# Kernel tuning notes

Measured on AMD Instinct MI355X. Metric: run time of the kernel, lower is better.

The kernel has to match this reference:

```python
import jax, jax.numpy as jnp
import numpy as np

N_KPS = 1024      # number of TPS control points
N_PTS = 120000    # number of query points to warp
RELAX = 0.5       # TPS relaxation (regularization on K diagonal)


def setup_inputs() -> dict:
    key = jax.random.key(0)
    k1, k2, k3 = jax.random.split(key, 3)
    # Control points in a [0,100)^2 coordinate frame.
    kps_a = jax.random.uniform(k1, (N_KPS, 2), dtype=jnp.float32) * 100.0
    kps_b = kps_a + jax.random.normal(k2, (N_KPS, 2), dtype=jnp.float32) * 2.0
    # --- replicate __init__: solve the TPS system for W ---
    d2 = jnp.sum((kps_a[:, None, :] - kps_a[None, :, :]) ** 2, axis=-1)  # [n_a, n_a]
    d2 = jnp.where(d2 == 0, 1.0, d2)
    K = 0.5 * d2 * jnp.log(d2) + RELAX * jnp.eye(N_KPS, dtype=jnp.float32)
    P = jnp.concatenate([jnp.ones((N_KPS, 1), jnp.float32), kps_a], axis=1)  # [n_a, 3]
    L = jnp.block([[K, P], [P.T, jnp.zeros((3, 3), jnp.float32)]])           # [n_a+3, n_a+3]
    v = jnp.concatenate([kps_b - kps_a, jnp.zeros((3, 2), jnp.float32)], axis=0)
    W = jnp.linalg.solve(L, v)  # [n_a+3, 2]  (equivalent to L.inverse() @ v)
    # Query points
    pts = jax.random.uniform(k3, (N_PTS, 2), dtype=jnp.float32) * 100.0
    return {"pts": pts, "kps_a": kps_a, "W": W}


def reference(pts, kps_a, W):
    # pairwise squared distances, [n_a, n_b] (matches __build_l2_mat)
    l2 = jnp.sum((kps_a[:, None, :] - pts[None, :, :]) ** 2, axis=-1)
    l2 = jnp.where(l2 == 0, 1.0, l2)
    v = 0.5 * l2 * jnp.log(l2)  # TPS radial basis r^2 * log(r)
    ones = jnp.ones_like(pts[:, 0])
    affine = jnp.stack([ones, pts[:, 0], pts[:, 1]], axis=0)   # [3, n_b]
    x = jnp.concatenate([v, affine], axis=0)                   # [n_a+3, n_b]
    z = x.T @ W                                                # [n_b, 2]
    return pts + z
```

## Files before the change

### kernel.cpp

```cpp
#include <hip/hip_runtime.h>

#define N_KPS 1024
#define N_PTS 120000
#define BLOCK 256
#define KSPLIT 4
#define KCHUNK (N_KPS / KSPLIT)
#define PTS_PER_BLOCK 128

typedef float v2f __attribute__((ext_vector_type(2)));

__global__ __launch_bounds__(BLOCK) void tps_warp_kernel(
    const float2* __restrict__ pts,
    const float*  __restrict__ kps,
    const float*  __restrict__ W,
    float2*       __restrict__ out)
{
    __shared__ float4 part[KSPLIT][64];

    const int lane = threadIdx.x & 63;
    const int kch  = threadIdx.x >> 6;
    const int base = blockIdx.x * PTS_PER_BLOCK;
    const int j0 = base + lane;
    const int j1 = base + 64 + lane;

    const int j0c = j0 < N_PTS ? j0 : N_PTS - 1;
    const int j1c = j1 < N_PTS ? j1 : N_PTS - 1;
    const float2 p0 = pts[j0c];
    const float2 p1 = pts[j1c];

    v2f px = {p0.x, p1.x};
    v2f py = {p0.y, p1.y};
    v2f zx = {0.0f, 0.0f};
    v2f zy = {0.0f, 0.0f};
    const v2f tiny = {1e-37f, 1e-37f};

    const int k0 = kch * KCHUNK;
    #pragma unroll 4
    for (int i = k0; i < k0 + KCHUNK; ++i) {
        float kx = kps[2 * i];
        float ky = kps[2 * i + 1];
        float wx = W[2 * i];
        float wy = W[2 * i + 1];
        v2f kxv = {kx, kx}, kyv = {ky, ky};
        v2f wxv = {wx, wx}, wyv = {wy, wy};

        v2f dx = kxv - px;
        v2f dy = kyv - py;
        v2f d2 = __builtin_elementwise_fma(dy, dy, dx * dx);
        d2 = __builtin_elementwise_max(d2, tiny);
        v2f t;
        t.x = __log2f(d2.x);
        t.y = __log2f(d2.y);
        v2f v = d2 * t;
        zx = __builtin_elementwise_fma(v, wxv, zx);
        zy = __builtin_elementwise_fma(v, wyv, zy);
    }

    part[kch][lane] = make_float4(zx.x, zy.x, zx.y, zy.y);
    __syncthreads();

    if (kch == 0) {
        float4 a = part[0][lane];
        float4 b = part[1][lane];
        float4 c = part[2][lane];
        float4 d = part[3][lane];
        float sx0 = (a.x + b.x) + (c.x + d.x);
        float sy0 = (a.y + b.y) + (c.y + d.y);
        float sx1 = (a.z + b.z) + (c.z + d.z);
        float sy1 = (a.w + b.w) + (c.w + d.w);

        const float scale = 0.34657359027997264f;
        float w1x = W[2048], w1y = W[2049];
        float wxx = W[2050], wxy = W[2051];
        float wyx = W[2052], wyy = W[2053];

        if (j0 < N_PTS) {
            float ox = p0.x + fmaf(scale, sx0, fmaf(wxx, p0.x, fmaf(wyx, p0.y, w1x)));
            float oy = p0.y + fmaf(scale, sy0, fmaf(wxy, p0.x, fmaf(wyy, p0.y, w1y)));
            out[j0] = make_float2(ox, oy);
        }
        if (j1 < N_PTS) {
            float ox = p1.x + fmaf(scale, sx1, fmaf(wxx, p1.x, fmaf(wyx, p1.y, w1x)));
            float oy = p1.y + fmaf(scale, sy1, fmaf(wxy, p1.x, fmaf(wyy, p1.y, w1y)));
            out[j1] = make_float2(ox, oy);
        }
    }
}

extern "C" void kernel_launch(void* const* d_in, const int* in_sizes, int n_in,
                              void* d_out, int out_size, void* d_ws, size_t ws_size,
                              hipStream_t stream) {
    const float* pts = (const float*)d_in[0];
    const float* kps = (const float*)d_in[1];
    const float* W   = (const float*)d_in[2];
    float* out = (float*)d_out;

    const int grid = (N_PTS + PTS_PER_BLOCK - 1) / PTS_PER_BLOCK;
    tps_warp_kernel<<<grid, BLOCK, 0, stream>>>(
        (const float2*)pts, kps, W, (float2*)out);
}
```

Measured before the change: 88.39 us.

## Split keypoints across 8 waves with wave-uniform float4 prefetched loads

Doubles the block to 512 threads so eight waves each handle 128 keypoints, and makes the wave index scalar via readfirstlane. Keypoint and weight data are now read as float4 vectors through scalar loads and double-buffered one chunk ahead of use, to cut per-iteration load latency and instruction count. The final reduction sums eight partial results instead of four. Larger blocks may lower occupancy flexibility and add more LDS reduction work per point.

```diff
diff --git a/kernel.cpp b/kernel.cpp
--- a/kernel.cpp
+++ b/kernel.cpp
@@ -2,10 +2,12 @@
 
 #define N_KPS 1024
 #define N_PTS 120000
-#define BLOCK 256
-#define KSPLIT 4
+#define BLOCK 512
+#define KSPLIT 8
 #define KCHUNK (N_KPS / KSPLIT)
 #define PTS_PER_BLOCK 128
+#define CHUNK 8
+#define NCHUNK (KCHUNK / CHUNK)
 
 typedef float v2f __attribute__((ext_vector_type(2)));
 
@@ -18,11 +20,11 @@
     __shared__ float4 part[KSPLIT][64];
 
     const int lane = threadIdx.x & 63;
-    const int kch  = threadIdx.x >> 6;
+    const int wv = __builtin_amdgcn_readfirstlane(threadIdx.x) >> 6;
+
     const int base = blockIdx.x * PTS_PER_BLOCK;
     const int j0 = base + lane;
     const int j1 = base + 64 + lane;
-
     const int j0c = j0 < N_PTS ? j0 : N_PTS - 1;
     const int j1c = j1 < N_PTS ? j1 : N_PTS - 1;
     const float2 p0 = pts[j0c];
@@ -34,40 +36,64 @@
     v2f zy = {0.0f, 0.0f};
     const v2f tiny = {1e-37f, 1e-37f};
 
-    const int k0 = kch * KCHUNK;
-    #pragma unroll 4
-    for (int i = k0; i < k0 + KCHUNK; ++i) {
-        float kx = kps[2 * i];
-        float ky = kps[2 * i + 1];
-        float wx = W[2 * i];
-        float wy = W[2 * i + 1];
-        v2f kxv = {kx, kx}, kyv = {ky, ky};
-        v2f wxv = {wx, wx}, wyv = {wy, wy};
-
-        v2f dx = kxv - px;
-        v2f dy = kyv - py;
+    auto eval = [&](float kx, float ky, float wx, float wy) {
+        v2f dx = v2f{kx, kx} - px;
+        v2f dy = v2f{ky, ky} - py;
         v2f d2 = __builtin_elementwise_fma(dy, dy, dx * dx);
         d2 = __builtin_elementwise_max(d2, tiny);
         v2f t;
         t.x = __log2f(d2.x);
         t.y = __log2f(d2.y);
         v2f v = d2 * t;
-        zx = __builtin_elementwise_fma(v, wxv, zx);
-        zy = __builtin_elementwise_fma(v, wyv, zy);
+        zx = __builtin_elementwise_fma(v, v2f{wx, wx}, zx);
+        zy = __builtin_elementwise_fma(v, v2f{wy, wy}, zy);
+    };
+
+    const float4* __restrict__ kp4 = (const float4*)kps;
+    const float4* __restrict__ wp4 = (const float4*)W;
+    const int cbase = wv * (KCHUNK / 2);
+
+    float4 kc[4], wc[4];
+    #pragma unroll
+    for (int t = 0; t < 4; ++t) {
+        kc[t] = kp4[cbase + t];
+        wc[t] = wp4[cbase + t];
     }
 
-    part[kch][lane] = make_float4(zx.x, zy.x, zx.y, zy.y);
+    for (int c = 0; c < NCHUNK; ++c) {
+        const int nc = (c + 1 < NCHUNK) ? c + 1 : c;
+        float4 kn[4], wn[4];
+        #pragma unroll
+        for (int t = 0; t < 4; ++t) {
+            kn[t] = kp4[cbase + nc * 4 + t];
+            wn[t] = wp4[cbase + nc * 4 + t];
+        }
+        #pragma unroll
+        for (int t = 0; t < 4; ++t) {
+            eval(kc[t].x, kc[t].y, wc[t].x, wc[t].y);
+            eval(kc[t].z, kc[t].w, wc[t].z, wc[t].w);
+        }
+        #pragma unroll
+        for (int t = 0; t < 4; ++t) {
+            kc[t] = kn[t];
+            wc[t] = wn[t];
+        }
+    }
+
+    part[wv][lane] = make_float4(zx.x, zy.x, zx.y, zy.y);
     __syncthreads();
 
-    if (kch == 0) {
-        float4 a = part[0][lane];
-        float4 b = part[1][lane];
-        float4 c = part[2][lane];
-        float4 d = part[3][lane];
-        float sx0 = (a.x + b.x) + (c.x + d.x);
-        float sy0 = (a.y + b.y) + (c.y + d.y);
-        float sx1 = (a.z + b.z) + (c.z + d.z);
-        float sy1 = (a.w + b.w) + (c.w + d.w);
+    if (wv == 0) {
+        float sx0 = 0.f, sy0 = 0.f, sx1 = 0.f, sy1 = 0.f;
+        #pragma unroll
+        for (int w = 0; w < KSPLIT; w += 2) {
+            float4 a = part[w][lane];
+            float4 b = part[w + 1][lane];
+            sx0 += a.x + b.x;
+            sy0 += a.y + b.y;
+            sx1 += a.z + b.z;
+            sy1 += a.w + b.w;
+        }
 
         const float scale = 0.34657359027997264f;
         float w1x = W[2048], w1y = W[2049];
```

Result: faster. 82.53 us (-6.6%).
